# Optimization experiments

Hardware: AMD Instinct MI355X
Metric: run time of the kernel (lower is better)

Reference implementation:

```python
import jax, jax.numpy as jnp
import numpy as np

B, N, C_X, D_MODEL, D_OUT, S = 32, 4096, 1, 64, 1, 2
D_IN = C_X + D_MODEL  # 65, channels entering graph_conv


def setup_inputs() -> dict:
    key = jax.random.key(0)
    ks = jax.random.split(key, 8)
    x = jax.random.normal(ks[0], (B, C_X, N), dtype=jnp.float32)
    h = jax.random.normal(ks[1], (B, D_MODEL, N), dtype=jnp.float32)
    # stacked support matrices (fwd/bwd normalized adjacency), used as a list of supports
    adj = jax.random.uniform(ks[2], (S, N, N), dtype=jnp.float32) / N
    # graph_conv.mlp : Conv2d(S*D_IN -> D_MODEL, 1x1)
    W_mlp = jax.random.normal(ks[3], (D_MODEL, S * D_IN), dtype=jnp.float32) / np.sqrt(S * D_IN)
    b_mlp = jnp.zeros((D_MODEL,), jnp.float32)
    # lin_out : Conv1d(2*D_MODEL -> D_MODEL, k=1)
    W_lin = jax.random.normal(ks[4], (D_MODEL, 2 * D_MODEL), dtype=jnp.float32) / np.sqrt(2 * D_MODEL)
    b_lin = jnp.zeros((D_MODEL,), jnp.float32)
    # read_out : Conv1d(2*D_MODEL -> D_OUT, k=1)
    W_read = jax.random.normal(ks[5], (D_OUT, 2 * D_MODEL), dtype=jnp.float32) / np.sqrt(2 * D_MODEL)
    b_read = jnp.zeros((D_OUT,), jnp.float32)
    prelu_a = jnp.array(0.25, jnp.float32)  # nn.PReLU() default: single shared slope
    return {"x": x, "h": h, "adj": adj, "W_mlp": W_mlp, "b_mlp": b_mlp,
            "W_lin": W_lin, "b_lin": b_lin, "W_read": W_read, "b_read": b_read,
            "prelu_a": prelu_a}


def conv1x1(W, b, x):
    # x: [B, C_in, N] -> [B, C_out, N]
    return jnp.einsum('oc,bcn->bon', W, x) + b[None, :, None]


def reference(x, h, adj, W_mlp, b_mlp, W_lin, b_lin, W_read, b_read, prelu_a):
    # x: [B, C_X, N], h: [B, D_MODEL, N], adj: [S, N, N]
    x_in = jnp.concatenate([x, h], axis=1)  # [B, D_IN, N]
    # SpatialConvOrderK (order=1, include_self=False):
    # out[b,c,w] per support s = sum_v x_in[b,c,v] * adj[s,w,v]
    hops = jnp.einsum('bcv,swv->bscw', x_in, adj)  # [B, S, D_IN, N]
    feats = hops.reshape(B, S * D_IN, N)           # channel-cat over supports
    out = conv1x1(W_mlp, b_mlp, feats)             # [B, D_MODEL, N]
    out = jnp.concatenate([out, h], axis=1)        # [B, 2*D_MODEL, N]
    out = conv1x1(W_lin, b_lin, out)               # [B, D_MODEL, N]
    out = jnp.where(out >= 0, out, prelu_a * out)  # PReLU
    out = jnp.concatenate([out, h], axis=1)        # [B, 2*D_MODEL, N]
    return (conv1x1(W_read, b_read, out), out)
```

## Files before the change

kernel.cpp:

```cpp
#include <hip/hip_runtime.h>
#include <cstdint>

#define N_NODES 4096
#define DM 64
#define K_DIM 8192
#define M_DIM 2048

typedef uint8_t u8;
using i32x8   = __attribute__((ext_vector_type(8))) int;
using floatx4 = __attribute__((ext_vector_type(4))) float;

#define GLOAD_LDS16(gp, lp)                                                     \
  __builtin_amdgcn_global_load_lds(                                             \
      reinterpret_cast<const __attribute__((address_space(1))) void*>(          \
          reinterpret_cast<uintptr_t>(gp)),                                     \
      reinterpret_cast<__attribute__((address_space(3))) void*>(                \
          (uint32_t)reinterpret_cast<uintptr_t>(lp)),                           \
      16, 0, 0)

__device__ inline int pk_fp8x4(float f0, float f1, float f2, float f3) {
  int r = __builtin_amdgcn_cvt_pk_fp8_f32(f0, f1, 0, false);
  r     = __builtin_amdgcn_cvt_pk_fp8_f32(f2, f3, r, true);
  return r;
}

__global__ __launch_bounds__(256) void k_prep(const float* __restrict__ adj,
                                              u8* __restrict__ BT8,
                                              const float* __restrict__ x,
                                              const float* __restrict__ h,
                                              const float* __restrict__ Wmlp,
                                              u8* __restrict__ A8) {
  __shared__ __align__(16) float Ws[DM * 68];
  uint32_t bi = blockIdx.x;
  if (bi < 16384u) {
    uint32_t idx = bi * 256u + threadIdx.x;
    uint32_t v8 = idx & 511u;
    uint32_t w  = (idx >> 9) & 4095u;
    uint32_t s  = idx >> 21;
    const float4* src = reinterpret_cast<const float4*>(adj) + (size_t)idx * 2;
    float4 f0 = src[0], f1 = src[1];
    uint2 pk;
    pk.x = (uint32_t)pk_fp8x4(f0.x * 4096.f, f0.y * 4096.f, f0.z * 4096.f, f0.w * 4096.f);
    pk.y = (uint32_t)pk_fp8x4(f1.x * 4096.f, f1.y * 4096.f, f1.z * 4096.f, f1.w * 4096.f);
    *reinterpret_cast<uint2*>(BT8 + ((size_t)w * K_DIM + s * N_NODES + v8 * 8)) = pk;
    return;
  }
  uint32_t b2 = bi - 16384u;
  uint32_t v0 = (b2 & 15u) * 256u;
  uint32_t s  = (b2 >> 4) & 1u;
  uint32_t b  = b2 >> 5;
  for (uint32_t t = threadIdx.x; t < DM * 68; t += 256) {
    uint32_t d = t / 68u, c = t % 68u;
    Ws[t] = (c < 65u) ? Wmlp[d * 130u + s * 65u + c] : 0.f;
  }
  __syncthreads();

  const uint32_t tv = threadIdx.x & 63u;
  const uint32_t td = threadIdx.x >> 6;
  const uint32_t v  = v0 + tv * 4u;

  float acc[16][4];
#pragma unroll
  for (int d = 0; d < 16; ++d)
#pragma unroll
    for (int k = 0; k < 4; ++k) acc[d][k] = 0.f;

  for (int c0 = 0; c0 < 64; c0 += 4) {
    float4 in4[4];
#pragma unroll
    for (int j = 0; j < 4; ++j) {
      int c = c0 + j;
      const float* src = (c == 0) ? (x + (size_t)b * N_NODES + v)
                                  : (h + ((size_t)b * DM + (c - 1)) * N_NODES + v);
      in4[j] = *reinterpret_cast<const float4*>(src);
    }
#pragma unroll
    for (int d = 0; d < 16; ++d) {
      const float4 w4 = *reinterpret_cast<const float4*>(&Ws[(td * 16 + d) * 68 + c0]);
      acc[d][0] += w4.x * in4[0].x + w4.y * in4[1].x + w4.z * in4[2].x + w4.w * in4[3].x;
      acc[d][1] += w4.x * in4[0].y + w4.y * in4[1].y + w4.z * in4[2].y + w4.w * in4[3].y;
      acc[d][2] += w4.x * in4[0].z + w4.y * in4[1].z + w4.z * in4[2].z + w4.w * in4[3].z;
      acc[d][3] += w4.x * in4[0].w + w4.y * in4[1].w + w4.z * in4[2].w + w4.w * in4[3].w;
    }
  }
  {
    float4 in4 = *reinterpret_cast<const float4*>(h + ((size_t)b * DM + 63) * N_NODES + v);
#pragma unroll
    for (int d = 0; d < 16; ++d) {
      float w = Ws[(td * 16 + d) * 68 + 64];
      acc[d][0] += w * in4.x; acc[d][1] += w * in4.y;
      acc[d][2] += w * in4.z; acc[d][3] += w * in4.w;
    }
  }
#pragma unroll
  for (int d = 0; d < 16; ++d) {
    int p = pk_fp8x4(acc[d][0], acc[d][1], acc[d][2], acc[d][3]);
    *reinterpret_cast<int*>(A8 + (size_t)(b * DM + td * 16 + d) * K_DIM + s * N_NODES + v) = p;
  }
}

__global__ void k_gemm(const u8* __restrict__ A, const u8* __restrict__ BT,
                       float* __restrict__ C) {
  __shared__ __align__(32) u8 As[4][128][32];
  __shared__ __align__(32) u8 Bs[4][128][32];
  const int tid  = threadIdx.x;
  const int lane = tid & 63;
  const int wave = tid >> 6;
  const int wr = wave >> 1, wc = wave & 1;
  const int m0 = blockIdx.y * 128, n0 = blockIdx.x * 128;
  const size_t kb = (size_t)blockIdx.z * 4096;

  const int srow = lane >> 1;
  const int shalf = (lane & 1) * 16;
  const u8* Ag = A  + (size_t)(m0 + wave * 32 + srow) * K_DIM + kb + shalf;
  const u8* Bg = BT + (size_t)(n0 + wave * 32 + srow) * K_DIM + kb + shalf;
  u8* AsB[4]; u8* BsB[4];
#pragma unroll
  for (int q = 0; q < 4; ++q) { AsB[q] = &As[q][wave * 32][0]; BsB[q] = &Bs[q][wave * 32][0]; }

  floatx4 acc[4][4];
#pragma unroll
  for (int i = 0; i < 4; ++i)
#pragma unroll
    for (int j = 0; j < 4; ++j) acc[i][j] = (floatx4){0.f, 0.f, 0.f, 0.f};

  const int fm = lane & 15;
  const int fq = lane >> 4;
  const int SC1 = 0x7F7F7F7F;

  for (int k0 = 0; k0 < 4096; k0 += 128) {
#pragma unroll
    for (int q = 0; q < 4; ++q) GLOAD_LDS16(Ag + k0 + q * 32, AsB[q]);
#pragma unroll
    for (int q = 0; q < 4; ++q) GLOAD_LDS16(Bg + k0 + q * 32, BsB[q]);
    __syncthreads();

    i32x8 af[4], bfr[4];
#pragma unroll
    for (int i = 0; i < 4; ++i)
      af[i] = *reinterpret_cast<const i32x8*>(&As[fq][wr * 64 + i * 16 + fm][0]);
#pragma unroll
    for (int j = 0; j < 4; ++j)
      bfr[j] = *reinterpret_cast<const i32x8*>(&Bs[fq][wc * 64 + j * 16 + fm][0]);
#pragma unroll
    for (int i = 0; i < 4; ++i)
#pragma unroll
      for (int j = 0; j < 4; ++j)
        acc[i][j] = __builtin_amdgcn_mfma_scale_f32_16x16x128_f8f6f4(
            af[i], bfr[j], acc[i][j], 0, 0, 0, SC1, 0, SC1);
    __syncthreads();
  }

  float* Cz = C + (size_t)blockIdx.z * M_DIM * N_NODES;
  const int cr = (lane >> 4) * 4;
  const int cc = lane & 15;
#pragma unroll
  for (int i = 0; i < 4; ++i)
#pragma unroll
    for (int j = 0; j < 4; ++j) {
      float* Cp = Cz + (size_t)(m0 + wr * 64 + i * 16 + cr) * N_NODES
                     + (n0 + wc * 64 + j * 16 + cc);
#pragma unroll
      for (int r = 0; r < 4; ++r) Cp[(size_t)r * N_NODES] = acc[i][j][r];
    }
}

__global__ __launch_bounds__(256) void k_epilogue(
    const float* __restrict__ C0, const float* __restrict__ C1,
    const float* __restrict__ h,
    const float* __restrict__ bmlp, const float* __restrict__ Wlin,
    const float* __restrict__ blin, const float* __restrict__ Wread,
    const float* __restrict__ bread, const float* __restrict__ pa,
    float* __restrict__ out0, float* __restrict__ out1) {
  __shared__ __align__(16) float sW[DM * 132];
  __shared__ float sbm[DM], sbl[DM], sWr[128];
  __shared__ float psum[3 * 256];
  for (uint32_t t = threadIdx.x; t < DM * 128; t += 256) {
    uint32_t d = t >> 7, c = t & 127u;
    sW[d * 132 + c] = Wlin[t];
  }
  if (threadIdx.x < DM) { sbm[threadIdx.x] = bmlp[threadIdx.x]; sbl[threadIdx.x] = blin[threadIdx.x]; }
  if (threadIdx.x < 128) sWr[threadIdx.x] = Wread[threadIdx.x];
  __syncthreads();

  uint32_t bi = blockIdx.x;
  uint32_t n0 = (bi & 15u) * 256u;
  uint32_t b  = bi >> 4;
  const uint32_t tv = threadIdx.x & 63u;
  const uint32_t td = threadIdx.x >> 6;
  const uint32_t n  = n0 + tv * 4u;
  const float KS = 1.0f / 4096.0f;

  float acc[16][4];
#pragma unroll
  for (int d = 0; d < 16; ++d) {
    float bl = sbl[td * 16 + d];
#pragma unroll
    for (int k = 0; k < 4; ++k) acc[d][k] = bl;
  }

  for (int c0 = 0; c0 < 64; c0 += 4) {
    float4 in4[4];
#pragma unroll
    for (int j = 0; j < 4; ++j) {
      size_t off = ((size_t)b * DM + (c0 + j)) * N_NODES + n;
      float4 v0 = *reinterpret_cast<const float4*>(C0 + off);
      float4 v1 = *reinterpret_cast<const float4*>(C1 + off);
      float bm = sbm[c0 + j];
      float4 v;
      v.x = (v0.x + v1.x) * KS + bm; v.y = (v0.y + v1.y) * KS + bm;
      v.z = (v0.z + v1.z) * KS + bm; v.w = (v0.w + v1.w) * KS + bm;
      in4[j] = v;
    }
#pragma unroll
    for (int d = 0; d < 16; ++d) {
      const float4 w4 = *reinterpret_cast<const float4*>(&sW[(td * 16 + d) * 132 + c0]);
      acc[d][0] += w4.x * in4[0].x + w4.y * in4[1].x + w4.z * in4[2].x + w4.w * in4[3].x;
      acc[d][1] += w4.x * in4[0].y + w4.y * in4[1].y + w4.z * in4[2].y + w4.w * in4[3].y;
      acc[d][2] += w4.x * in4[0].z + w4.y * in4[1].z + w4.z * in4[2].z + w4.w * in4[3].z;
      acc[d][3] += w4.x * in4[0].w + w4.y * in4[1].w + w4.z * in4[2].w + w4.w * in4[3].w;
    }
  }
  for (int c0 = 0; c0 < 64; c0 += 4) {
    float4 in4[4];
#pragma unroll
    for (int j = 0; j < 4; ++j)
      in4[j] = *reinterpret_cast<const float4*>(h + ((size_t)b * DM + (c0 + j)) * N_NODES + n);
#pragma unroll
    for (int d = 0; d < 16; ++d) {
      const float4 w4 = *reinterpret_cast<const float4*>(&sW[(td * 16 + d) * 132 + 64 + c0]);
      acc[d][0] += w4.x * in4[0].x + w4.y * in4[1].x + w4.z * in4[2].x + w4.w * in4[3].x;
      acc[d][1] += w4.x * in4[0].y + w4.y * in4[1].y + w4.z * in4[2].y + w4.w * in4[3].y;
      acc[d][2] += w4.x * in4[0].z + w4.y * in4[1].z + w4.z * in4[2].z + w4.w * in4[3].z;
      acc[d][3] += w4.x * in4[0].w + w4.y * in4[1].w + w4.z * in4[2].w + w4.w * in4[3].w;
    }
  }

  const float a = pa[0];
  float r[4] = {0.f, 0.f, 0.f, 0.f};
  float* o1b = out1 + (size_t)b * 128 * N_NODES + n;
#pragma unroll
  for (int d = 0; d < 16; ++d) {
    float4 o2;
    o2.x = acc[d][0] >= 0.f ? acc[d][0] : a * acc[d][0];
    o2.y = acc[d][1] >= 0.f ? acc[d][1] : a * acc[d][1];
    o2.z = acc[d][2] >= 0.f ? acc[d][2] : a * acc[d][2];
    o2.w = acc[d][3] >= 0.f ? acc[d][3] : a * acc[d][3];
    *reinterpret_cast<float4*>(o1b + (size_t)(td * 16 + d) * N_NODES) = o2;
    float wr = sWr[td * 16 + d];
    r[0] += wr * o2.x; r[1] += wr * o2.y; r[2] += wr * o2.z; r[3] += wr * o2.w;
  }
#pragma unroll
  for (int d = 0; d < 16; ++d) {
    float4 hv = *reinterpret_cast<const float4*>(h + ((size_t)b * DM + td * 16 + d) * N_NODES + n);
    *reinterpret_cast<float4*>(o1b + (size_t)(64 + td * 16 + d) * N_NODES) = hv;
    float wr = sWr[64 + td * 16 + d];
    r[0] += wr * hv.x; r[1] += wr * hv.y; r[2] += wr * hv.z; r[3] += wr * hv.w;
  }
  if (td > 0) {
#pragma unroll
    for (int k = 0; k < 4; ++k) psum[(td - 1) * 256 + tv * 4 + k] = r[k];
  }
  __syncthreads();
  if (td == 0) {
    float br = bread[0];
#pragma unroll
    for (int k = 0; k < 4; ++k)
      r[k] += br + psum[tv * 4 + k] + psum[256 + tv * 4 + k] + psum[512 + tv * 4 + k];
    float4 o0; o0.x = r[0]; o0.y = r[1]; o0.z = r[2]; o0.w = r[3];
    *reinterpret_cast<float4*>(out0 + (size_t)b * N_NODES + n) = o0;
  }
}

extern "C" void kernel_launch(void* const* d_in, const int* in_sizes, int n_in,
                              void* d_out, int out_size, void* d_ws, size_t ws_size,
                              hipStream_t stream) {
  const float* x     = (const float*)d_in[0];
  const float* h     = (const float*)d_in[1];
  const float* adj   = (const float*)d_in[2];
  const float* Wmlp  = (const float*)d_in[3];
  const float* bmlp  = (const float*)d_in[4];
  const float* Wlin  = (const float*)d_in[5];
  const float* blin  = (const float*)d_in[6];
  const float* Wread = (const float*)d_in[7];
  const float* bread = (const float*)d_in[8];
  const float* pa    = (const float*)d_in[9];

  char* ws = (char*)d_ws;
  u8*    Abuf  = (u8*)ws;
  u8*    BTbuf = (u8*)(ws + (16ull << 20));
  float* C0    = (float*)(ws + (48ull << 20));
  float* C1    = (float*)(ws + (80ull << 20));
  float* out0 = (float*)d_out;
  float* out1 = out0 + 131072;

  hipLaunchKernelGGL(k_prep,     dim3(17408),     dim3(256), 0, stream,
                     adj, BTbuf, x, h, Wmlp, Abuf);
  hipLaunchKernelGGL(k_gemm,     dim3(32, 16, 2), dim3(256), 0, stream, Abuf, BTbuf, C0);
  hipLaunchKernelGGL(k_epilogue, dim3(512),       dim3(256), 0, stream, C0, C1, h, bmlp,
                     Wlin, blin, Wread, bread, pa, out0, out1);
}
```

Before: 422.9 us.

## Fold W_lin into W_mlp to drop one epilogue matmul stage

Adds a tiny single-block kernel that precomputes W_lin[:, :64] @ W_mlp and the matching combined bias, then uses the folded weights when building the fp8 A operand. The epilogue now starts from the GEMM result plus the folded bias and only applies the h half of W_lin, which removes a 64x64 per-node matmul. The old prep kernel is split into separate adjacency-conversion and A-building kernels, adding launches, and the extra kernel serializes ahead of the rest.

```diff
diff --git a/kernel.cpp b/kernel.cpp
--- a/kernel.cpp
+++ b/kernel.cpp
@@ -24,34 +24,61 @@
   return r;
 }
 
-__global__ __launch_bounds__(256) void k_prep(const float* __restrict__ adj,
-                                              u8* __restrict__ BT8,
-                                              const float* __restrict__ x,
-                                              const float* __restrict__ h,
-                                              const float* __restrict__ Wmlp,
-                                              u8* __restrict__ A8) {
+__global__ __launch_bounds__(256) void k_fold(const float* __restrict__ Wmlp,
+                                              const float* __restrict__ bmlp,
+                                              const float* __restrict__ Wlin,
+                                              const float* __restrict__ blin,
+                                              float* __restrict__ WLW,
+                                              float* __restrict__ b2) {
+  __shared__ float sWl[64 * 64];
+  __shared__ float sWm[64 * 130];
+  for (uint32_t t = threadIdx.x; t < 64 * 128; t += 256) {
+    uint32_t d = t >> 7, c = t & 127u;
+    if (c < 64u) sWl[d * 64 + c] = Wlin[t];
+  }
+  for (uint32_t t = threadIdx.x; t < 64 * 130; t += 256) sWm[t] = Wmlp[t];
+  __syncthreads();
+  for (uint32_t o = threadIdx.x; o < 64 * 130; o += 256) {
+    uint32_t dp = o / 130u, sc = o % 130u;
+    float s = 0.f;
+#pragma unroll 8
+    for (int d = 0; d < 64; ++d) s += sWl[dp * 64 + d] * sWm[d * 130 + sc];
+    WLW[o] = s;
+  }
+  if (threadIdx.x < 64) {
+    float s = blin[threadIdx.x];
+#pragma unroll 8
+    for (int d = 0; d < 64; ++d) s += sWl[threadIdx.x * 64 + d] * bmlp[d];
+    b2[threadIdx.x] = s;
+  }
+}
+
+__global__ __launch_bounds__(256) void k_adj2bt(const float* __restrict__ adj,
+                                                u8* __restrict__ BT8) {
+  uint32_t idx = blockIdx.x * 256u + threadIdx.x;
+  uint32_t v8 = idx & 511u;
+  uint32_t w  = (idx >> 9) & 4095u;
+  uint32_t s  = idx >> 21;
+  const float4* src = reinterpret_cast<const float4*>(adj) + (size_t)idx * 2;
+  float4 f0 = src[0], f1 = src[1];
+  uint2 pk;
+  pk.x = (uint32_t)pk_fp8x4(f0.x * 4096.f, f0.y * 4096.f, f0.z * 4096.f, f0.w * 4096.f);
+  pk.y = (uint32_t)pk_fp8x4(f1.x * 4096.f, f1.y * 4096.f, f1.z * 4096.f, f1.w * 4096.f);
+  *reinterpret_cast<uint2*>(BT8 + ((size_t)w * K_DIM + s * N_NODES + v8 * 8)) = pk;
+}
+
+__global__ __launch_bounds__(256) void k_mkA(const float* __restrict__ x,
+                                             const float* __restrict__ h,
+                                             const float* __restrict__ WLW,
+                                             u8* __restrict__ A8) {
   __shared__ __align__(16) float Ws[DM * 68];
   uint32_t bi = blockIdx.x;
-  if (bi < 16384u) {
-    uint32_t idx = bi * 256u + threadIdx.x;
-    uint32_t v8 = idx & 511u;
-    uint32_t w  = (idx >> 9) & 4095u;
-    uint32_t s  = idx >> 21;
-    const float4* src = reinterpret_cast<const float4*>(adj) + (size_t)idx * 2;
-    float4 f0 = src[0], f1 = src[1];
-    uint2 pk;
-    pk.x = (uint32_t)pk_fp8x4(f0.x * 4096.f, f0.y * 4096.f, f0.z * 4096.f, f0.w * 4096.f);
-    pk.y = (uint32_t)pk_fp8x4(f1.x * 4096.f, f1.y * 4096.f, f1.z * 4096.f, f1.w * 4096.f);
-    *reinterpret_cast<uint2*>(BT8 + ((size_t)w * K_DIM + s * N_NODES + v8 * 8)) = pk;
-    return;
-  }
-  uint32_t b2 = bi - 16384u;
-  uint32_t v0 = (b2 & 15u) * 256u;
-  uint32_t s  = (b2 >> 4) & 1u;
-  uint32_t b  = b2 >> 5;
+  uint32_t v0 = (bi & 15u) * 256u;
+  uint32_t s  = (bi >> 4) & 1u;
+  uint32_t b  = bi >> 5;
   for (uint32_t t = threadIdx.x; t < DM * 68; t += 256) {
     uint32_t d = t / 68u, c = t % 68u;
-    Ws[t] = (c < 65u) ? Wmlp[d * 130u + s * 65u + c] : 0.f;
+    Ws[t] = (c < 65u) ? WLW[d * 130u + s * 65u + c] : 0.f;
   }
   __syncthreads();
 
@@ -167,19 +194,18 @@
 
 __global__ __launch_bounds__(256) void k_epilogue(
     const float* __restrict__ C0, const float* __restrict__ C1,
-    const float* __restrict__ h,
-    const float* __restrict__ bmlp, const float* __restrict__ Wlin,
-    const float* __restrict__ blin, const float* __restrict__ Wread,
+    const float* __restrict__ h, const float* __restrict__ Wlin,
+    const float* __restrict__ b2g, const float* __restrict__ Wread,
     const float* __restrict__ bread, const float* __restrict__ pa,
     float* __restrict__ out0, float* __restrict__ out1) {
-  __shared__ __align__(16) float sW[DM * 132];
-  __shared__ float sbm[DM], sbl[DM], sWr[128];
+  __shared__ __align__(16) float sWb[DM * 68];
+  __shared__ float sb2[DM], sWr[128];
   __shared__ float psum[3 * 256];
-  for (uint32_t t = threadIdx.x; t < DM * 128; t += 256) {
-    uint32_t d = t >> 7, c = t & 127u;
-    sW[d * 132 + c] = Wlin[t];
-  }
-  if (threadIdx.x < DM) { sbm[threadIdx.x] = bmlp[threadIdx.x]; sbl[threadIdx.x] = blin[threadIdx.x]; }
+  for (uint32_t t = threadIdx.x; t < DM * 64; t += 256) {
+    uint32_t d = t >> 6, c = t & 63u;
+    sWb[d * 68 + c] = Wlin[d * 128 + 64 + c];
+  }
+  if (threadIdx.x < DM) sb2[threadIdx.x] = b2g[threadIdx.x];
   if (threadIdx.x < 128) sWr[threadIdx.x] = Wread[threadIdx.x];
   __syncthreads();
 
@@ -194,41 +220,24 @@
   float acc[16][4];
 #pragma unroll
   for (int d = 0; d < 16; ++d) {
-    float bl = sbl[td * 16 + d];
-#pragma unroll
-    for (int k = 0; k < 4; ++k) acc[d][k] = bl;
+    size_t off = ((size_t)b * DM + td * 16 + d) * N_NODES + n;
+    float4 v0 = *reinterpret_cast<const float4*>(C0 + off);
+    float4 v1 = *reinterpret_cast<const float4*>(C1 + off);
+    float bb = sb2[td * 16 + d];
+    acc[d][0] = (v0.x + v1.x) * KS + bb;
+    acc[d][1] = (v0.y + v1.y) * KS + bb;
+    acc[d][2] = (v0.z + v1.z) * KS + bb;
+    acc[d][3] = (v0.w + v1.w) * KS + bb;
   }
 
   for (int c0 = 0; c0 < 64; c0 += 4) {
     float4 in4[4];
 #pragma unroll
-    for (int j = 0; j < 4; ++j) {
-      size_t off = ((size_t)b * DM + (c0 + j)) * N_NODES + n;
-      float4 v0 = *reinterpret_cast<const float4*>(C0 + off);
-      float4 v1 = *reinterpret_cast<const float4*>(C1 + off);
-      float bm = sbm[c0 + j];
-      float4 v;
-      v.x = (v0.x + v1.x) * KS + bm; v.y = (v0.y + v1.y) * KS + bm;
-      v.z = (v0.z + v1.z) * KS + bm; v.w = (v0.w + v1.w) * KS + bm;
-      in4[j] = v;
-    }
-#pragma unroll
-    for (int d = 0; d < 16; ++d) {
-      const float4 w4 = *reinterpret_cast<const float4*>(&sW[(td * 16 + d) * 132 + c0]);
-      acc[d][0] += w4.x * in4[0].x + w4.y * in4[1].x + w4.z * in4[2].x + w4.w * in4[3].x;
-      acc[d][1] += w4.x * in4[0].y + w4.y * in4[1].y + w4.z * in4[2].y + w4.w * in4[3].y;
-      acc[d][2] += w4.x * in4[0].z + w4.y * in4[1].z + w4.z * in4[2].z + w4.w * in4[3].z;
-      acc[d][3] += w4.x * in4[0].w + w4.y * in4[1].w + w4.z * in4[2].w + w4.w * in4[3].w;
-    }
-  }
-  for (int c0 = 0; c0 < 64; c0 += 4) {
-    float4 in4[4];
-#pragma unroll
     for (int j = 0; j < 4; ++j)
       in4[j] = *reinterpret_cast<const float4*>(h + ((size_t)b * DM + (c0 + j)) * N_NODES + n);
 #pragma unroll
     for (int d = 0; d < 16; ++d) {
-      const float4 w4 = *reinterpret_cast<const float4*>(&sW[(td * 16 + d) * 132 + 64 + c0]);
+      const float4 w4 = *reinterpret_cast<const float4*>(&sWb[(td * 16 + d) * 68 + c0]);
       acc[d][0] += w4.x * in4[0].x + w4.y * in4[1].x + w4.z * in4[2].x + w4.w * in4[3].x;
       acc[d][1] += w4.x * in4[0].y + w4.y * in4[1].y + w4.z * in4[2].y + w4.w * in4[3].y;
       acc[d][2] += w4.x * in4[0].z + w4.y * in4[1].z + w4.z * in4[2].z + w4.w * in4[3].z;
@@ -289,14 +298,18 @@
   char* ws = (char*)d_ws;
   u8*    Abuf  = (u8*)ws;
   u8*    BTbuf = (u8*)(ws + (16ull << 20));
-  float* C0    = (float*)(ws + (48ull << 20));
-  float* C1    = (float*)(ws + (80ull << 20));
+  float* Cbuf  = (float*)(ws + (48ull << 20));
+  float* WLW   = (float*)(ws + (112ull << 20));
+  float* b2    = (float*)(ws + (112ull << 20) + 65536);
   float* out0 = (float*)d_out;
   float* out1 = out0 + 131072;
 
-  hipLaunchKernelGGL(k_prep,     dim3(17408),     dim3(256), 0, stream,
-                     adj, BTbuf, x, h, Wmlp, Abuf);
-  hipLaunchKernelGGL(k_gemm,     dim3(32, 16, 2), dim3(256), 0, stream, Abuf, BTbuf, C0);
-  hipLaunchKernelGGL(k_epilogue, dim3(512),       dim3(256), 0, stream, C0, C1, h, bmlp,
-                     Wlin, blin, Wread, bread, pa, out0, out1);
-}
+  hipLaunchKernelGGL(k_fold,     dim3(1),         dim3(256), 0, stream,
+                     Wmlp, bmlp, Wlin, blin, WLW, b2);
+  hipLaunchKernelGGL(k_adj2bt,   dim3(16384),     dim3(256), 0, stream, adj, BTbuf);
+  hipLaunchKernelGGL(k_mkA,      dim3(1024),      dim3(256), 0, stream, x, h, WLW, Abuf);
+  hipLaunchKernelGGL(k_gemm,     dim3(32, 16, 2), dim3(256), 0, stream, Abuf, BTbuf, Cbuf);
+  hipLaunchKernelGGL(k_epilogue, dim3(512),       dim3(256), 0, stream,
+                     Cbuf, Cbuf + (size_t)M_DIM * N_NODES, h, Wlin, b2,
+                     Wread, bread, pa, out0, out1);
+}
```

After: 449.7 us. 1.06x slower.
